# Kernel optimization log

Measured on AMD Instinct MI355X. Metric: run time of the kernel, lower is better.

Reference implementation:

```python
import jax, jax.numpy as jnp
import numpy as np

N_NODES = 50000
N_EDGES = 1600000
N_FEAT = 50
HID = 20
OUT_DIM = 10
N_GRAPHS = 64


def _glorot(key, shape):
    fan_in, fan_out = shape[0], shape[1]
    lim = float(np.sqrt(6.0 / (fan_in + fan_out)))
    return jax.random.uniform(key, shape, jnp.float32, -lim, lim)


def setup_inputs() -> dict:
    key = jax.random.key(0)
    ks = jax.random.split(key, 16)
    x = jax.random.normal(ks[0], (N_NODES, N_FEAT), jnp.float32)
    edge_index = jax.random.randint(ks[1], (2, N_EDGES), 0, N_NODES, jnp.int32)
    batch = jnp.sort(jax.random.randint(ks[2], (N_NODES,), 0, N_GRAPHS, jnp.int32))
    inp = {"x": x, "edge_index": edge_index, "batch": batch}
    # GraphConv layer params: lin_rel (weight+bias, applied to aggregated msgs), lin_root (no bias)
    dims = [(N_FEAT, HID), (HID, HID), (HID, HID)]
    for i, (di, do) in enumerate(dims, start=1):
        inp[f"W_rel{i}"] = _glorot(ks[3 * i], (di, do))
        inp[f"W_root{i}"] = _glorot(ks[3 * i + 1], (di, do))
        inp[f"b{i}"] = jnp.zeros((do,), jnp.float32)
    # final Linear on cat([max_pool, mean_pool]) -> in_features = 2*HID
    inp["W_lin"] = _glorot(ks[13], (2 * HID, OUT_DIM))
    inp["b_lin"] = jnp.zeros((OUT_DIM,), jnp.float32)
    return inp


def _graph_conv(x, src, dst, W_rel, W_root, b):
    # PyG GraphConv: aggregate raw neighbor features (sum), then linear.
    agg = jax.ops.segment_sum(x[src], dst, num_segments=N_NODES)  # [N, d_in]
    return agg @ W_rel + x @ W_root + b


def reference(x, edge_index, batch,
              W_rel1, W_root1, b1,
              W_rel2, W_root2, b2,
              W_rel3, W_root3, b3,
              W_lin, b_lin):
    src, dst = edge_index[0], edge_index[1]
    h = jax.nn.relu(_graph_conv(x, src, dst, W_rel1, W_root1, b1))
    h = jax.nn.relu(_graph_conv(h, src, dst, W_rel2, W_root2, b2))
    h = jax.nn.relu(_graph_conv(h, src, dst, W_rel3, W_root3, b3))
    # global max / mean pool per graph
    maxP = jax.ops.segment_max(h, batch, num_segments=N_GRAPHS)  # [G, HID]
    sums = jax.ops.segment_sum(h, batch, num_segments=N_GRAPHS)
    cnt = jax.ops.segment_sum(jnp.ones((h.shape[0], 1), h.dtype), batch, num_segments=N_GRAPHS)
    meanP = sums / jnp.maximum(cnt, 1.0)
    return jnp.concatenate([maxP, meanP], axis=-1) @ W_lin + b_lin
```

## Files before the change

### kernel.cpp

```cpp
#include <hip/hip_runtime.h>

#define N_NODES  50000
#define N_EDGES  1600000
#define N_FEAT   50
#define HID      20
#define OUT_DIM  10
#define N_GRAPHS 64

#define NBUCK 256
#define BCAP  8192
#define EPB   (N_EDGES/256)
#define YSTR  32
#define GEMMB 977

__device__ __forceinline__ int bstart(int b) { return (b * 65536 + 334) / 335; }


__global__ __launch_bounds__(1024) void k1_scatter_gemm(
        const int* __restrict__ dst, const int* __restrict__ srcv,
        int* __restrict__ gcur, unsigned int* __restrict__ padded,
        const float* __restrict__ x, const float* __restrict__ Wrel,
        const float* __restrict__ Wroot, const float* __restrict__ bb,
        float* __restrict__ y, float* __restrict__ acc,
        float* __restrict__ gmax, float* __restrict__ gsum, float* __restrict__ gcnt) {
    __shared__ char smem[14560];
    int t = threadIdx.x;
    if (blockIdx.x < 256) {
        unsigned short* rnk = (unsigned short*)smem;
        int* cnt   = (int*)(smem + 12512);
        int* gbase = cnt + 256;
        if (blockIdx.x == 0) {
            for (int i = t; i < N_GRAPHS * HID; i += 1024) { gmax[i] = 0.f; gsum[i] = 0.f; }
            if (t < N_GRAPHS) gcnt[t] = 0.f;
        }
        if (t < 256) cnt[t] = 0;
        __syncthreads();
        int e0 = blockIdx.x * EPB;
        for (int i = t; i < EPB; i += 1024) {
            unsigned int d = (unsigned int)dst[e0 + i];
            unsigned int key = (d * 335u) >> 16;
            rnk[i] = (unsigned short)atomicAdd(&cnt[key], 1);
        }
        __syncthreads();
        if (t < 256) gbase[t] = t * BCAP + atomicAdd(&gcur[t], cnt[t]);
        __syncthreads();
        for (int i = t; i < EPB; i += 1024) {
            unsigned int d = (unsigned int)dst[e0 + i];
            unsigned int s = (unsigned int)srcv[e0 + i];
            unsigned int key = (d * 335u) >> 16;
            int gp = gbase[key] + rnk[i];
            if (gp < (int)(key + 1) * BCAP) padded[gp] = (d << 16) | s;
        }
    } else {
        float* sWrel  = (float*)smem;
        float* sWroot = sWrel + N_FEAT * HID;
        for (int i = t; i < N_FEAT * HID; i += 1024) { sWrel[i] = Wrel[i]; sWroot[i] = Wroot[i]; }
        __syncthreads();
        int idx = (blockIdx.x - 256) * 1024 + t;
        if (idx < N_NODES * HID) {
            int n = idx / HID, j = idx % HID;
            const float* xr = x + n * N_FEAT;
            float a0 = 0.f, a1 = bb[j];
            #pragma unroll
            for (int k = 0; k < N_FEAT; ++k) {
                float xv = xr[k];
                a0 = fmaf(xv, sWrel[k * HID + j], a0);
                a1 = fmaf(xv, sWroot[k * HID + j], a1);
            }
            y[n * YSTR + j] = a0;
            acc[idx] = a1;
        }
    }
}


__global__ __launch_bounds__(1024) void k2_build_gather(
        const int* __restrict__ gcur, const unsigned int* __restrict__ padded,
        unsigned short* __restrict__ csr16, int* __restrict__ startg,
        int* __restrict__ cntg, unsigned short* __restrict__ permg,
        const float* __restrict__ y_in, const float* __restrict__ accp,
        const float* __restrict__ Wrel, const float* __restrict__ Wroot,
        const float* __restrict__ bb,
        float* __restrict__ y_out, float* __restrict__ acc_out) {
    __shared__ unsigned short eo[BCAP];
    __shared__ char uni[20480];
    __shared__ float sWrel[HID * HID], sWroot[HID * HID], sb[HID];
    __shared__ int cnt[256], scn[256], s_start[256], s_cnt[256];
    __shared__ unsigned short sperm[256];
    unsigned short* rnk = (unsigned short*)uni;
    float*          rh  = (float*)uni;
    int g = blockIdx.x, t = threadIdx.x;
    int base = g * BCAP;
    int m = min(gcur[g], BCAP);
    int n0 = bstart(g);
    int n1 = min(bstart(g + 1), N_NODES);
    int nvalid = n1 - n0;
    for (int i = t; i < HID * HID; i += 1024) { sWrel[i] = Wrel[i]; sWroot[i] = Wroot[i]; }
    if (t < HID) sb[t] = bb[t];
    if (t < 256) cnt[t] = 0;
    __syncthreads();
    for (int i = t; i < m; i += 1024) {
        int local = (int)(padded[base + i] >> 16) - n0;
        rnk[i] = (unsigned short)atomicAdd(&cnt[local], 1);
    }
    __syncthreads();
    if (t < 256) { s_cnt[t] = cnt[t]; scn[t] = cnt[t]; }
    __syncthreads();
    for (int d = 1; d < 256; d <<= 1) {
        int u = 0;
        if (t < 256 && t >= d) u = scn[t - d];
        __syncthreads();
        if (t < 256) scn[t] += u;
        __syncthreads();
    }
    if (t < 256) {
        s_start[t] = scn[t] - s_cnt[t];
        if (t < nvalid) { startg[n0 + t] = base + s_start[t]; cntg[n0 + t] = s_cnt[t]; }
    }
    __syncthreads();
    for (int i = t; i < m; i += 1024) {
        unsigned int e = padded[base + i];
        int local = (int)(e >> 16) - n0;
        eo[s_start[local] + rnk[i]] = (unsigned short)(e & 0xFFFFu);
    }
    __syncthreads();
    for (int i = t; i < m; i += 1024) csr16[base + i] = eo[i];
    if (t < 256) {
        int d = s_cnt[t], rank = 0;
        for (int j2 = 0; j2 < 256; ++j2) {
            int dj = s_cnt[j2];
            rank += (dj > d) || (dj == d && j2 < t);
        }
        sperm[rank] = (unsigned short)t;
    }
    __syncthreads();
    if (t < 256) permg[g * 256 + t] = sperm[t];
    for (int i = t; i < nvalid * HID; i += 1024) rh[i] = accp[n0 * HID + i];
    __syncthreads();
    int grp = t >> 3, lane = t & 7;
    if (lane < 5) {
        int q4 = lane * 4;
        #pragma unroll
        for (int rep = 0; rep < 2; ++rep) {
            int rank = rep ? 255 - grp : grp;
            int nl = sperm[rank];
            if (nl < nvalid) {
                int a = s_start[nl], e = a + s_cnt[nl];
                float4 s0 = make_float4(0.f, 0.f, 0.f, 0.f);
                float4 s1 = make_float4(0.f, 0.f, 0.f, 0.f);
                int k = a;
                for (; k + 3 < e; k += 4) {
                    int sn0 = eo[k], sn1 = eo[k + 1], sn2 = eo[k + 2], sn3 = eo[k + 3];
                    float4 v0 = *(const float4*)(y_in + sn0 * YSTR + q4);
                    float4 v1 = *(const float4*)(y_in + sn1 * YSTR + q4);
                    float4 v2 = *(const float4*)(y_in + sn2 * YSTR + q4);
                    float4 v3 = *(const float4*)(y_in + sn3 * YSTR + q4);
                    s0.x += v0.x + v2.x; s0.y += v0.y + v2.y;
                    s0.z += v0.z + v2.z; s0.w += v0.w + v2.w;
                    s1.x += v1.x + v3.x; s1.y += v1.y + v3.y;
                    s1.z += v1.z + v3.z; s1.w += v1.w + v3.w;
                }
                for (; k < e; ++k) {
                    int sn = eo[k];
                    float4 v = *(const float4*)(y_in + sn * YSTR + q4);
                    s0.x += v.x; s0.y += v.y; s0.z += v.z; s0.w += v.w;
                }
                float* rp = &rh[nl * HID + q4];
                rp[0] += s0.x + s1.x; rp[1] += s0.y + s1.y;
                rp[2] += s0.z + s1.z; rp[3] += s0.w + s1.w;
            }
        }
    }
    __syncthreads();
    for (int i = t; i < nvalid * 5; i += 1024) {
        int n = i / 5, j0 = (i % 5) * 4;
        float y0 = 0.f, y1 = 0.f, y2 = 0.f, y3 = 0.f;
        float a0 = sb[j0], a1 = sb[j0 + 1], a2 = sb[j0 + 2], a3 = sb[j0 + 3];
        #pragma unroll
        for (int k = 0; k < HID; ++k) {
            float h = fmaxf(rh[n * HID + k], 0.f);
            const float* wr = sWrel  + k * HID + j0;
            const float* wo = sWroot + k * HID + j0;
            y0 = fmaf(h, wr[0], y0); y1 = fmaf(h, wr[1], y1);
            y2 = fmaf(h, wr[2], y2); y3 = fmaf(h, wr[3], y3);
            a0 = fmaf(h, wo[0], a0); a1 = fmaf(h, wo[1], a1);
            a2 = fmaf(h, wo[2], a2); a3 = fmaf(h, wo[3], a3);
        }
        *(float4*)(y_out   + (n0 + n) * YSTR + j0) = make_float4(y0, y1, y2, y3);
        *(float4*)(acc_out + (n0 + n) * HID  + j0) = make_float4(a0, a1, a2, a3);
    }
}


__global__ __launch_bounds__(1024) void k3_gather_gemm(
        const int* __restrict__ startg, const int* __restrict__ cntg,
        const unsigned short* __restrict__ csr16, const unsigned short* __restrict__ permg,
        const float* __restrict__ y_in, const float* __restrict__ accp,
        const float* __restrict__ Wrel, const float* __restrict__ Wroot,
        const float* __restrict__ bb,
        float* __restrict__ y_out, float* __restrict__ acc_out) {
    __shared__ float rh[256 * HID];
    __shared__ float sWrel[HID * HID], sWroot[HID * HID], sb[HID];
    int g = blockIdx.x, t = threadIdx.x;
    int n0 = bstart(g);
    int n1 = min(bstart(g + 1), N_NODES);
    int nvalid = n1 - n0;
    for (int i = t; i < HID * HID; i += 1024) { sWrel[i] = Wrel[i]; sWroot[i] = Wroot[i]; }
    if (t < HID) sb[t] = bb[t];
    for (int i = t; i < nvalid * HID; i += 1024) rh[i] = accp[n0 * HID + i];
    __syncthreads();
    int grp = t >> 3, lane = t & 7;
    if (lane < 5) {
        int q4 = lane * 4;
        #pragma unroll
        for (int rep = 0; rep < 2; ++rep) {
            int rank = rep ? 255 - grp : grp;
            int nl = permg[g * 256 + rank];
            if (nl < nvalid) {
                int node = n0 + nl;
                int a = startg[node], e = a + cntg[node];
                float4 s0 = make_float4(0.f, 0.f, 0.f, 0.f);
                float4 s1 = make_float4(0.f, 0.f, 0.f, 0.f);
                int k = a;
                for (; k + 3 < e; k += 4) {
                    int sn0 = csr16[k], sn1 = csr16[k + 1], sn2 = csr16[k + 2], sn3 = csr16[k + 3];
                    float4 v0 = *(const float4*)(y_in + sn0 * YSTR + q4);
                    float4 v1 = *(const float4*)(y_in + sn1 * YSTR + q4);
                    float4 v2 = *(const float4*)(y_in + sn2 * YSTR + q4);
                    float4 v3 = *(const float4*)(y_in + sn3 * YSTR + q4);
                    s0.x += v0.x + v2.x; s0.y += v0.y + v2.y;
                    s0.z += v0.z + v2.z; s0.w += v0.w + v2.w;
                    s1.x += v1.x + v3.x; s1.y += v1.y + v3.y;
                    s1.z += v1.z + v3.z; s1.w += v1.w + v3.w;
                }
                for (; k < e; ++k) {
                    int sn = csr16[k];
                    float4 v = *(const float4*)(y_in + sn * YSTR + q4);
                    s0.x += v.x; s0.y += v.y; s0.z += v.z; s0.w += v.w;
                }
                float* rp = &rh[nl * HID + q4];
                rp[0] += s0.x + s1.x; rp[1] += s0.y + s1.y;
                rp[2] += s0.z + s1.z; rp[3] += s0.w + s1.w;
            }
        }
    }
    __syncthreads();
    for (int i = t; i < nvalid * 5; i += 1024) {
        int n = i / 5, j0 = (i % 5) * 4;
        float y0 = 0.f, y1 = 0.f, y2 = 0.f, y3 = 0.f;
        float a0 = sb[j0], a1 = sb[j0 + 1], a2 = sb[j0 + 2], a3 = sb[j0 + 3];
        #pragma unroll
        for (int k = 0; k < HID; ++k) {
            float h = fmaxf(rh[n * HID + k], 0.f);
            const float* wr = sWrel  + k * HID + j0;
            const float* wo = sWroot + k * HID + j0;
            y0 = fmaf(h, wr[0], y0); y1 = fmaf(h, wr[1], y1);
            y2 = fmaf(h, wr[2], y2); y3 = fmaf(h, wr[3], y3);
            a0 = fmaf(h, wo[0], a0); a1 = fmaf(h, wo[1], a1);
            a2 = fmaf(h, wo[2], a2); a3 = fmaf(h, wo[3], a3);
        }
        *(float4*)(y_out   + (n0 + n) * YSTR + j0) = make_float4(y0, y1, y2, y3);
        *(float4*)(acc_out + (n0 + n) * HID  + j0) = make_float4(a0, a1, a2, a3);
    }
}


__global__ __launch_bounds__(1024) void k4_gather_pool(
        const int* __restrict__ startg, const int* __restrict__ cntg,
        const unsigned short* __restrict__ csr16, const unsigned short* __restrict__ permg,
        const float* __restrict__ y_in, const float* __restrict__ accp,
        const int* __restrict__ batch,
        float* __restrict__ gmax, float* __restrict__ gsum, float* __restrict__ gcnt,
        int* __restrict__ done, const float* __restrict__ Wlin,
        const float* __restrict__ blin, float* __restrict__ out) {
    __shared__ float rh[256 * HID];
    __shared__ float redm[51 * HID], reds[51 * HID];
    __shared__ int sbatch[256];
    __shared__ int seglo[16], seghi[16];
    __shared__ int lastFlag;
    int g = blockIdx.x, t = threadIdx.x;
    int n0 = bstart(g);
    int n1 = min(bstart(g + 1), N_NODES);
    int nvalid = n1 - n0;
    for (int i = t; i < nvalid * HID; i += 1024) rh[i] = accp[n0 * HID + i];
    if (t < nvalid) sbatch[t] = batch[n0 + t];
    __syncthreads();
    int grp = t >> 3, lane = t & 7;
    if (lane < 5) {
        int q4 = lane * 4;
        #pragma unroll
        for (int rep = 0; rep < 2; ++rep) {
            int rank = rep ? 255 - grp : grp;
            int nl = permg[g * 256 + rank];
            if (nl < nvalid) {
                int node = n0 + nl;
                int a = startg[node], e = a + cntg[node];
                float4 s0 = make_float4(0.f, 0.f, 0.f, 0.f);
                float4 s1 = make_float4(0.f, 0.f, 0.f, 0.f);
                int k = a;
                for (; k + 3 < e; k += 4) {
                    int sn0 = csr16[k], sn1 = csr16[k + 1], sn2 = csr16[k + 2], sn3 = csr16[k + 3];
                    float4 v0 = *(const float4*)(y_in + sn0 * YSTR + q4);
                    float4 v1 = *(const float4*)(y_in + sn1 * YSTR + q4);
                    float4 v2 = *(const float4*)(y_in + sn2 * YSTR + q4);
                    float4 v3 = *(const float4*)(y_in + sn3 * YSTR + q4);
                    s0.x += v0.x + v2.x; s0.y += v0.y + v2.y;
                    s0.z += v0.z + v2.z; s0.w += v0.w + v2.w;
                    s1.x += v1.x + v3.x; s1.y += v1.y + v3.y;
                    s1.z += v1.z + v3.z; s1.w += v1.w + v3.w;
                }
                for (; k < e; ++k) {
                    int sn = csr16[k];
                    float4 v = *(const float4*)(y_in + sn * YSTR + q4);
                    s0.x += v.x; s0.y += v.y; s0.z += v.z; s0.w += v.w;
                }
                float* rp = &rh[nl * HID + q4];
                rp[0] += s0.x + s1.x; rp[1] += s0.y + s1.y;
                rp[2] += s0.z + s1.z; rp[3] += s0.w + s1.w;
            }
        }
    }
    __syncthreads();
    int g0 = sbatch[0];
    int span = sbatch[nvalid - 1] - g0 + 1;
    if (t < nvalid) {
        int bi = sbatch[t] - g0;
        if (bi < 16) {
            if (t == 0 || sbatch[t - 1] != sbatch[t]) seglo[bi] = t;
            if (t == nvalid - 1 || sbatch[t + 1] != sbatch[t]) seghi[bi] = t + 1;
        }
    }
    __syncthreads();
    if (span > 16) span = 16;
    for (int li = 0; li < span; ++li) {
        int lo = seglo[li], hi = seghi[li];
        int r = t / HID, j = t % HID;
        if (r < 51) {
            float mx = 0.f, sm = 0.f;
            for (int n = lo + r; n < hi; n += 51) {
                float v = fmaxf(rh[n * HID + j], 0.f);
                mx = fmaxf(mx, v); sm += v;
            }
            redm[r * HID + j] = mx; reds[r * HID + j] = sm;
        }
        __syncthreads();
        if (t < HID) {
            float mm = 0.f, ss = 0.f;
            #pragma unroll 17
            for (int r2 = 0; r2 < 51; ++r2) {
                mm = fmaxf(mm, redm[r2 * HID + t]);
                ss += reds[r2 * HID + t];
            }
            atomicMax((int*)&gmax[(g0 + li) * HID + t], __float_as_int(mm));
            atomicAdd(&gsum[(g0 + li) * HID + t], ss);
        }
        if (t == HID) atomicAdd(&gcnt[g0 + li], (float)(hi - lo));
        __syncthreads();
    }
    if (t == 0) {
        __threadfence();
        lastFlag = (atomicAdd(done, 1) == NBUCK - 1);
    }
    __syncthreads();
    if (!lastFlag) return;
    __threadfence();
    float* sW = redm;
    for (int i = t; i < 2 * HID * OUT_DIM; i += 1024) sW[i] = Wlin[i];
    __syncthreads();
    if (t < N_GRAPHS * OUT_DIM) {
        int gg = t / OUT_DIM, o = t % OUT_DIM;
        float c = fmaxf(gcnt[gg], 1.0f);
        float a = blin[o];
        #pragma unroll
        for (int j = 0; j < HID; ++j) {
            a = fmaf(gmax[gg * HID + j], sW[j * OUT_DIM + o], a);
            a = fmaf(gsum[gg * HID + j] / c, sW[(HID + j) * OUT_DIM + o], a);
        }
        out[t] = a;
    }
}

extern "C" void kernel_launch(void* const* d_in, const int* in_sizes, int n_in,
                              void* d_out, int out_size, void* d_ws, size_t ws_size,
                              hipStream_t stream) {
    const float* x      = (const float*)d_in[0];
    const int*   ei     = (const int*)  d_in[1];
    const int*   batch  = (const int*)  d_in[2];
    const float* Wrel1  = (const float*)d_in[3];
    const float* Wroot1 = (const float*)d_in[4];
    const float* b1     = (const float*)d_in[5];
    const float* Wrel2  = (const float*)d_in[6];
    const float* Wroot2 = (const float*)d_in[7];
    const float* b2     = (const float*)d_in[8];
    const float* Wrel3  = (const float*)d_in[9];
    const float* Wroot3 = (const float*)d_in[10];
    const float* b3     = (const float*)d_in[11];
    const float* Wlin   = (const float*)d_in[12];
    const float* blin   = (const float*)d_in[13];
    float* out = (float*)d_out;

    char* ws = (char*)d_ws;
    const size_t YB = (size_t)N_NODES * YSTR * sizeof(float);
    const size_t AB = (size_t)N_NODES * HID * sizeof(float);
    const size_t PB = (size_t)NBUCK * BCAP * sizeof(int);
    const size_t CB = (size_t)NBUCK * BCAP * sizeof(unsigned short);
    float*          yA     = (float*)(ws);
    float*          yB     = (float*)(ws + YB);
    float*          accA   = (float*)(ws + 2 * YB);
    float*          accB   = (float*)(ws + 2 * YB + AB);
    unsigned int*   padded = (unsigned int*)(ws + 2 * YB + 2 * AB);
    unsigned short* csr16  = (unsigned short*)(ws + 2 * YB + 2 * AB + PB);
    int*            startg = (int*)(ws + 2 * YB + 2 * AB + PB + CB);
    int*            cntg   = startg + N_NODES;
    unsigned short* permg  = (unsigned short*)(cntg + N_NODES);
    int*            gcur   = (int*)((char*)permg + (size_t)NBUCK * 256 * 2);
    int*            done   = gcur + NBUCK;
    float*          gmax   = (float*)(done + 4);
    float*          gsum   = gmax + N_GRAPHS * HID;
    float*          gcnt   = gsum + N_GRAPHS * HID;

    const int* src = ei;
    const int* dst = ei + N_EDGES;

    hipMemsetAsync(gcur, 0, (NBUCK + 1) * sizeof(int), stream);
    k1_scatter_gemm<<<256 + GEMMB, 1024, 0, stream>>>(dst, src, gcur, padded,
                                                      x, Wrel1, Wroot1, b1, yA, accA,
                                                      gmax, gsum, gcnt);
    k2_build_gather<<<NBUCK, 1024, 0, stream>>>(gcur, padded, csr16, startg, cntg, permg,
                                                yA, accA, Wrel2, Wroot2, b2, yB, accB);
    k3_gather_gemm<<<NBUCK, 1024, 0, stream>>>(startg, cntg, csr16, permg,
                                               yB, accB, Wrel3, Wroot3, b3, yA, accA);
    k4_gather_pool<<<NBUCK, 1024, 0, stream>>>(startg, cntg, csr16, permg,
                                               yA, accA, batch, gmax, gsum, gcnt,
                                               done, Wlin, blin, out);
}
```

Measured before the change: 122.3 us.

## Store gathered features as bf16, bucket by dst>>8, widen per-node gather threads

Intermediate y features used in neighbour gathers are now stored as bf16 (packed 20 values per row) instead of fp32, which halves the bytes read per edge in the gather kernels. Bucketing switches from a multiply-shift hash to plain 256-node buckets (dst>>8), with 196 buckets and a larger capacity. The scatter step first sorts edges locally in shared memory so global writes to the padded buffer are contiguous. The gather is restructured so each node's full 20-wide row is accumulated by 2 or 4 threads that split the edge list, with a shared-memory reduction afterwards. The cost is bf16 rounding error in the aggregated messages and more register pressure from the 20-float accumulator per thread.

```diff
diff --git a/kernel.cpp b/kernel.cpp
--- a/kernel.cpp
+++ b/kernel.cpp
@@ -7,13 +7,35 @@
 #define OUT_DIM  10
 #define N_GRAPHS 64
 
-#define NBUCK 256
-#define BCAP  8192
-#define EPB   (N_EDGES/256)
+#define NBUCK 196
+#define BCAP  10240
+#define EPB   6250
 #define YSTR  32
 #define GEMMB 977
 
-__device__ __forceinline__ int bstart(int b) { return (b * 65536 + 334) / 335; }
+__device__ __forceinline__ unsigned short f2bf(float f) {
+    unsigned int u = __float_as_uint(f);
+    u += 0x7FFFu + ((u >> 16) & 1u);
+    return (unsigned short)(u >> 16);
+}
+__device__ __forceinline__ unsigned int pk2(float f0, float f1) {
+    return (unsigned int)f2bf(f0) | ((unsigned int)f2bf(f1) << 16);
+}
+__device__ __forceinline__ float blo(unsigned int u) { return __uint_as_float(u << 16); }
+__device__ __forceinline__ float bhi(unsigned int u) { return __uint_as_float(u & 0xFFFF0000u); }
+
+__device__ __forceinline__ void addrow(const unsigned short* __restrict__ yb,
+                                       int sn, float* a) {
+    const unsigned short* p = yb + (size_t)sn * YSTR;
+    uint4 q0 = *(const uint4*)(p);
+    uint4 q1 = *(const uint4*)(p + 8);
+    uint2 q2 = *(const uint2*)(p + 16);
+    a[0] += blo(q0.x); a[1] += bhi(q0.x); a[2] += blo(q0.y); a[3] += bhi(q0.y);
+    a[4] += blo(q0.z); a[5] += bhi(q0.z); a[6] += blo(q0.w); a[7] += bhi(q0.w);
+    a[8] += blo(q1.x); a[9] += bhi(q1.x); a[10] += blo(q1.y); a[11] += bhi(q1.y);
+    a[12] += blo(q1.z); a[13] += bhi(q1.z); a[14] += blo(q1.w); a[15] += bhi(q1.w);
+    a[16] += blo(q2.x); a[17] += bhi(q2.x); a[18] += blo(q2.y); a[19] += bhi(q2.y);
+}
 
 
 __global__ __launch_bounds__(1024) void k1_scatter_gemm(
@@ -21,14 +43,17 @@
         int* __restrict__ gcur, unsigned int* __restrict__ padded,
         const float* __restrict__ x, const float* __restrict__ Wrel,
         const float* __restrict__ Wroot, const float* __restrict__ bb,
-        float* __restrict__ y, float* __restrict__ acc,
+        unsigned short* __restrict__ y, float* __restrict__ acc,
         float* __restrict__ gmax, float* __restrict__ gsum, float* __restrict__ gcnt) {
-    __shared__ char smem[14560];
+    __shared__ char smem[41728];
     int t = threadIdx.x;
     if (blockIdx.x < 256) {
         unsigned short* rnk = (unsigned short*)smem;
-        int* cnt   = (int*)(smem + 12512);
-        int* gbase = cnt + 256;
+        unsigned int*   ep2 = (unsigned int*)(smem + 12544);
+        int* cnt   = (int*)(smem + 37632);
+        int* scn   = cnt + 256;
+        int* lofs  = scn + 256;
+        int* gbase = lofs + 256;
         if (blockIdx.x == 0) {
             for (int i = t; i < N_GRAPHS * HID; i += 1024) { gmax[i] = 0.f; gsum[i] = 0.f; }
             if (t < N_GRAPHS) gcnt[t] = 0.f;
@@ -37,19 +62,33 @@
         __syncthreads();
         int e0 = blockIdx.x * EPB;
         for (int i = t; i < EPB; i += 1024) {
-            unsigned int d = (unsigned int)dst[e0 + i];
-            unsigned int key = (d * 335u) >> 16;
-            rnk[i] = (unsigned short)atomicAdd(&cnt[key], 1);
-        }
-        __syncthreads();
-        if (t < 256) gbase[t] = t * BCAP + atomicAdd(&gcur[t], cnt[t]);
+            int d = dst[e0 + i];
+            rnk[i] = (unsigned short)atomicAdd(&cnt[d >> 8], 1);
+        }
+        __syncthreads();
+        if (t < 256) scn[t] = cnt[t];
+        __syncthreads();
+        for (int d = 1; d < 256; d <<= 1) {
+            int u = 0;
+            if (t < 256 && t >= d) u = scn[t - d];
+            __syncthreads();
+            if (t < 256) scn[t] += u;
+            __syncthreads();
+        }
+        if (t < 256) lofs[t] = scn[t] - cnt[t];
+        if (t < NBUCK) gbase[t] = t * BCAP + atomicAdd(&gcur[t], cnt[t]);
         __syncthreads();
         for (int i = t; i < EPB; i += 1024) {
             unsigned int d = (unsigned int)dst[e0 + i];
             unsigned int s = (unsigned int)srcv[e0 + i];
-            unsigned int key = (d * 335u) >> 16;
-            int gp = gbase[key] + rnk[i];
-            if (gp < (int)(key + 1) * BCAP) padded[gp] = (d << 16) | s;
+            ep2[lofs[d >> 8] + rnk[i]] = (d << 16) | s;
+        }
+        __syncthreads();
+        for (int i = t; i < EPB; i += 1024) {
+            unsigned int e = ep2[i];
+            int bk = e >> 24;
+            int gp = gbase[bk] + (i - lofs[bk]);
+            if (gp < (bk + 1) * BCAP) padded[gp] = e;
         }
     } else {
         float* sWrel  = (float*)smem;
@@ -67,7 +106,7 @@
                 a0 = fmaf(xv, sWrel[k * HID + j], a0);
                 a1 = fmaf(xv, sWroot[k * HID + j], a1);
             }
-            y[n * YSTR + j] = a0;
+            y[(size_t)n * YSTR + j] = f2bf(a0);
             acc[idx] = a1;
         }
     }
@@ -78,10 +117,10 @@
         const int* __restrict__ gcur, const unsigned int* __restrict__ padded,
         unsigned short* __restrict__ csr16, int* __restrict__ startg,
         int* __restrict__ cntg, unsigned short* __restrict__ permg,
-        const float* __restrict__ y_in, const float* __restrict__ accp,
+        const unsigned short* __restrict__ y_in, const float* __restrict__ accp,
         const float* __restrict__ Wrel, const float* __restrict__ Wroot,
         const float* __restrict__ bb,
-        float* __restrict__ y_out, float* __restrict__ acc_out) {
+        unsigned short* __restrict__ y_out, float* __restrict__ acc_out) {
     __shared__ unsigned short eo[BCAP];
     __shared__ char uni[20480];
     __shared__ float sWrel[HID * HID], sWroot[HID * HID], sb[HID];
@@ -92,15 +131,14 @@
     int g = blockIdx.x, t = threadIdx.x;
     int base = g * BCAP;
     int m = min(gcur[g], BCAP);
-    int n0 = bstart(g);
-    int n1 = min(bstart(g + 1), N_NODES);
-    int nvalid = n1 - n0;
+    int n0 = g * 256;
+    int nvalid = min(256, N_NODES - n0);
     for (int i = t; i < HID * HID; i += 1024) { sWrel[i] = Wrel[i]; sWroot[i] = Wroot[i]; }
     if (t < HID) sb[t] = bb[t];
     if (t < 256) cnt[t] = 0;
     __syncthreads();
     for (int i = t; i < m; i += 1024) {
-        int local = (int)(padded[base + i] >> 16) - n0;
+        int local = (padded[base + i] >> 16) & 255;
         rnk[i] = (unsigned short)atomicAdd(&cnt[local], 1);
     }
     __syncthreads();
@@ -120,7 +158,7 @@
     __syncthreads();
     for (int i = t; i < m; i += 1024) {
         unsigned int e = padded[base + i];
-        int local = (int)(e >> 16) - n0;
+        int local = (e >> 16) & 255;
         eo[s_start[local] + rnk[i]] = (unsigned short)(e & 0xFFFFu);
     }
     __syncthreads();
@@ -135,47 +173,49 @@
     }
     __syncthreads();
     if (t < 256) permg[g * 256 + t] = sperm[t];
-    for (int i = t; i < nvalid * HID; i += 1024) rh[i] = accp[n0 * HID + i];
-    __syncthreads();
-    int grp = t >> 3, lane = t & 7;
-    if (lane < 5) {
-        int q4 = lane * 4;
-        #pragma unroll
-        for (int rep = 0; rep < 2; ++rep) {
-            int rank = rep ? 255 - grp : grp;
-            int nl = sperm[rank];
-            if (nl < nvalid) {
-                int a = s_start[nl], e = a + s_cnt[nl];
-                float4 s0 = make_float4(0.f, 0.f, 0.f, 0.f);
-                float4 s1 = make_float4(0.f, 0.f, 0.f, 0.f);
-                int k = a;
-                for (; k + 3 < e; k += 4) {
-                    int sn0 = eo[k], sn1 = eo[k + 1], sn2 = eo[k + 2], sn3 = eo[k + 3];
-                    float4 v0 = *(const float4*)(y_in + sn0 * YSTR + q4);
-                    float4 v1 = *(const float4*)(y_in + sn1 * YSTR + q4);
-                    float4 v2 = *(const float4*)(y_in + sn2 * YSTR + q4);
-                    float4 v3 = *(const float4*)(y_in + sn3 * YSTR + q4);
-                    s0.x += v0.x + v2.x; s0.y += v0.y + v2.y;
-                    s0.z += v0.z + v2.z; s0.w += v0.w + v2.w;
-                    s1.x += v1.x + v3.x; s1.y += v1.y + v3.y;
-                    s1.z += v1.z + v3.z; s1.w += v1.w + v3.w;
-                }
-                for (; k < e; ++k) {
-                    int sn = eo[k];
-                    float4 v = *(const float4*)(y_in + sn * YSTR + q4);
-                    s0.x += v.x; s0.y += v.y; s0.z += v.z; s0.w += v.w;
-                }
-                float* rp = &rh[nl * HID + q4];
-                rp[0] += s0.x + s1.x; rp[1] += s0.y + s1.y;
-                rp[2] += s0.z + s1.z; rp[3] += s0.w + s1.w;
-            }
+    bool act = t < 512;
+    int slot = t >> 1, half = t & 1;
+    float a[HID];
+    #pragma unroll
+    for (int j = 0; j < HID; ++j) a[j] = 0.f;
+    int nl = 0; bool ok = false; int a0 = 0, cn = 0;
+    if (act) {
+        nl = sperm[slot];
+        ok = nl < nvalid;
+        if (ok) { a0 = s_start[nl]; cn = s_cnt[nl]; }
+    }
+    if (ok) {
+        #pragma unroll 2
+        for (int k = half; k < cn; k += 2) addrow(y_in, eo[a0 + k], a);
+        if (half == 0) {
+            const float4* ar = (const float4*)(accp + (size_t)(n0 + nl) * HID);
+            #pragma unroll
+            for (int q = 0; q < 5; ++q) {
+                float4 v = ar[q];
+                a[q*4+0] += v.x; a[q*4+1] += v.y; a[q*4+2] += v.z; a[q*4+3] += v.w;
+            }
+        }
+    }
+    if (ok && half == 0) {
+        #pragma unroll
+        for (int q = 0; q < 5; ++q)
+            *(float4*)&rh[nl * HID + q * 4] =
+                make_float4(a[q*4], a[q*4+1], a[q*4+2], a[q*4+3]);
+    }
+    __syncthreads();
+    if (ok && half == 1) {
+        #pragma unroll
+        for (int q = 0; q < 5; ++q) {
+            float4 v = *(float4*)&rh[nl * HID + q * 4];
+            v.x += a[q*4]; v.y += a[q*4+1]; v.z += a[q*4+2]; v.w += a[q*4+3];
+            *(float4*)&rh[nl * HID + q * 4] = v;
         }
     }
     __syncthreads();
     for (int i = t; i < nvalid * 5; i += 1024) {
         int n = i / 5, j0 = (i % 5) * 4;
         float y0 = 0.f, y1 = 0.f, y2 = 0.f, y3 = 0.f;
-        float a0 = sb[j0], a1 = sb[j0 + 1], a2 = sb[j0 + 2], a3 = sb[j0 + 3];
+        float c0 = sb[j0], c1 = sb[j0+1], c2 = sb[j0+2], c3 = sb[j0+3];
         #pragma unroll
         for (int k = 0; k < HID; ++k) {
             float h = fmaxf(rh[n * HID + k], 0.f);
@@ -183,11 +223,11 @@
             const float* wo = sWroot + k * HID + j0;
             y0 = fmaf(h, wr[0], y0); y1 = fmaf(h, wr[1], y1);
             y2 = fmaf(h, wr[2], y2); y3 = fmaf(h, wr[3], y3);
-            a0 = fmaf(h, wo[0], a0); a1 = fmaf(h, wo[1], a1);
-            a2 = fmaf(h, wo[2], a2); a3 = fmaf(h, wo[3], a3);
-        }
-        *(float4*)(y_out   + (n0 + n) * YSTR + j0) = make_float4(y0, y1, y2, y3);
-        *(float4*)(acc_out + (n0 + n) * HID  + j0) = make_float4(a0, a1, a2, a3);
+            c0 = fmaf(h, wo[0], c0); c1 = fmaf(h, wo[1], c1);
+            c2 = fmaf(h, wo[2], c2); c3 = fmaf(h, wo[3], c3);
+        }
+        *(uint2*)(y_out + (size_t)(n0 + n) * YSTR + j0) = make_uint2(pk2(y0, y1), pk2(y2, y3));
+        *(float4*)(acc_out + (size_t)(n0 + n) * HID + j0) = make_float4(c0, c1, c2, c3);
     }
 }
 
@@ -195,72 +235,75 @@
 __global__ __launch_bounds__(1024) void k3_gather_gemm(
         const int* __restrict__ startg, const int* __restrict__ cntg,
         const unsigned short* __restrict__ csr16, const unsigned short* __restrict__ permg,
-        const float* __restrict__ y_in, const float* __restrict__ accp,
+        const unsigned short* __restrict__ y_in, const float* __restrict__ accp,
         const float* __restrict__ Wrel, const float* __restrict__ Wroot,
         const float* __restrict__ bb,
-        float* __restrict__ y_out, float* __restrict__ acc_out) {
+        unsigned short* __restrict__ y_out, float* __restrict__ acc_out) {
     __shared__ float rh[256 * HID];
+    __shared__ float rh2[256 * HID];
     __shared__ float sWrel[HID * HID], sWroot[HID * HID], sb[HID];
+    __shared__ unsigned short sperm[256];
     int g = blockIdx.x, t = threadIdx.x;
-    int n0 = bstart(g);
-    int n1 = min(bstart(g + 1), N_NODES);
-    int nvalid = n1 - n0;
+    int n0 = g * 256;
+    int nvalid = min(256, N_NODES - n0);
     for (int i = t; i < HID * HID; i += 1024) { sWrel[i] = Wrel[i]; sWroot[i] = Wroot[i]; }
     if (t < HID) sb[t] = bb[t];
-    for (int i = t; i < nvalid * HID; i += 1024) rh[i] = accp[n0 * HID + i];
-    __syncthreads();
-    int grp = t >> 3, lane = t & 7;
-    if (lane < 5) {
-        int q4 = lane * 4;
-        #pragma unroll
-        for (int rep = 0; rep < 2; ++rep) {
-            int rank = rep ? 255 - grp : grp;
-            int nl = permg[g * 256 + rank];
-            if (nl < nvalid) {
-                int node = n0 + nl;
-                int a = startg[node], e = a + cntg[node];
-                float4 s0 = make_float4(0.f, 0.f, 0.f, 0.f);
-                float4 s1 = make_float4(0.f, 0.f, 0.f, 0.f);
-                int k = a;
-                for (; k + 3 < e; k += 4) {
-                    int sn0 = csr16[k], sn1 = csr16[k + 1], sn2 = csr16[k + 2], sn3 = csr16[k + 3];
-                    float4 v0 = *(const float4*)(y_in + sn0 * YSTR + q4);
-                    float4 v1 = *(const float4*)(y_in + sn1 * YSTR + q4);
-                    float4 v2 = *(const float4*)(y_in + sn2 * YSTR + q4);
-                    float4 v3 = *(const float4*)(y_in + sn3 * YSTR + q4);
-                    s0.x += v0.x + v2.x; s0.y += v0.y + v2.y;
-                    s0.z += v0.z + v2.z; s0.w += v0.w + v2.w;
-                    s1.x += v1.x + v3.x; s1.y += v1.y + v3.y;
-                    s1.z += v1.z + v3.z; s1.w += v1.w + v3.w;
-                }
-                for (; k < e; ++k) {
-                    int sn = csr16[k];
-                    float4 v = *(const float4*)(y_in + sn * YSTR + q4);
-                    s0.x += v.x; s0.y += v.y; s0.z += v.z; s0.w += v.w;
-                }
-                float* rp = &rh[nl * HID + q4];
-                rp[0] += s0.x + s1.x; rp[1] += s0.y + s1.y;
-                rp[2] += s0.z + s1.z; rp[3] += s0.w + s1.w;
-            }
+    if (t < 256) sperm[t] = permg[g * 256 + t];
+    __syncthreads();
+    int slot = t >> 2, q = t & 3;
+    int nl = sperm[slot];
+    bool ok = nl < nvalid;
+    float a[HID];
+    #pragma unroll
+    for (int j = 0; j < HID; ++j) a[j] = 0.f;
+    if (ok) {
+        int node = n0 + nl;
+        int a0 = startg[node], cn = cntg[node];
+        #pragma unroll 2
+        for (int k = q; k < cn; k += 4) addrow(y_in, csr16[a0 + k], a);
+        if (q == 0) {
+            const float4* ar = (const float4*)(accp + (size_t)node * HID);
+            #pragma unroll
+            for (int qq = 0; qq < 5; ++qq) {
+                float4 v = ar[qq];
+                a[qq*4+0] += v.x; a[qq*4+1] += v.y; a[qq*4+2] += v.z; a[qq*4+3] += v.w;
+            }
+        }
+    }
+    if (ok && (q == 0 || q == 2)) {
+        float* dstp = (q == 0) ? rh : rh2;
+        #pragma unroll
+        for (int qq = 0; qq < 5; ++qq)
+            *(float4*)&dstp[nl * HID + qq * 4] =
+                make_float4(a[qq*4], a[qq*4+1], a[qq*4+2], a[qq*4+3]);
+    }
+    __syncthreads();
+    if (ok && (q == 1 || q == 3)) {
+        float* dstp = (q == 1) ? rh : rh2;
+        #pragma unroll
+        for (int qq = 0; qq < 5; ++qq) {
+            float4 v = *(float4*)&dstp[nl * HID + qq * 4];
+            v.x += a[qq*4]; v.y += a[qq*4+1]; v.z += a[qq*4+2]; v.w += a[qq*4+3];
+            *(float4*)&dstp[nl * HID + qq * 4] = v;
         }
     }
     __syncthreads();
     for (int i = t; i < nvalid * 5; i += 1024) {
         int n = i / 5, j0 = (i % 5) * 4;
         float y0 = 0.f, y1 = 0.f, y2 = 0.f, y3 = 0.f;
-        float a0 = sb[j0], a1 = sb[j0 + 1], a2 = sb[j0 + 2], a3 = sb[j0 + 3];
+        float c0 = sb[j0], c1 = sb[j0+1], c2 = sb[j0+2], c3 = sb[j0+3];
         #pragma unroll
         for (int k = 0; k < HID; ++k) {
-            float h = fmaxf(rh[n * HID + k], 0.f);
+            float h = fmaxf(rh[n * HID + k] + rh2[n * HID + k], 0.f);
             const float* wr = sWrel  + k * HID + j0;
             const float* wo = sWroot + k * HID + j0;
             y0 = fmaf(h, wr[0], y0); y1 = fmaf(h, wr[1], y1);
             y2 = fmaf(h, wr[2], y2); y3 = fmaf(h, wr[3], y3);
-            a0 = fmaf(h, wo[0], a0); a1 = fmaf(h, wo[1], a1);
-            a2 = fmaf(h, wo[2], a2); a3 = fmaf(h, wo[3], a3);
-        }
-        *(float4*)(y_out   + (n0 + n) * YSTR + j0) = make_float4(y0, y1, y2, y3);
-        *(float4*)(acc_out + (n0 + n) * HID  + j0) = make_float4(a0, a1, a2, a3);
+            c0 = fmaf(h, wo[0], c0); c1 = fmaf(h, wo[1], c1);
+            c2 = fmaf(h, wo[2], c2); c3 = fmaf(h, wo[3], c3);
+        }
+        *(uint2*)(y_out + (size_t)(n0 + n) * YSTR + j0) = make_uint2(pk2(y0, y1), pk2(y2, y3));
+        *(float4*)(acc_out + (size_t)(n0 + n) * HID + j0) = make_float4(c0, c1, c2, c3);
     }
 }
 
@@ -268,56 +311,59 @@
 __global__ __launch_bounds__(1024) void k4_gather_pool(
         const int* __restrict__ startg, const int* __restrict__ cntg,
         const unsigned short* __restrict__ csr16, const unsigned short* __restrict__ permg,
-        const float* __restrict__ y_in, const float* __restrict__ accp,
+        const unsigned short* __restrict__ y_in, const float* __restrict__ accp,
         const int* __restrict__ batch,
         float* __restrict__ gmax, float* __restrict__ gsum, float* __restrict__ gcnt,
         int* __restrict__ done, const float* __restrict__ Wlin,
         const float* __restrict__ blin, float* __restrict__ out) {
     __shared__ float rh[256 * HID];
+    __shared__ float rh2[256 * HID];
     __shared__ float redm[51 * HID], reds[51 * HID];
+    __shared__ unsigned short sperm[256];
     __shared__ int sbatch[256];
     __shared__ int seglo[16], seghi[16];
     __shared__ int lastFlag;
     int g = blockIdx.x, t = threadIdx.x;
-    int n0 = bstart(g);
-    int n1 = min(bstart(g + 1), N_NODES);
-    int nvalid = n1 - n0;
-    for (int i = t; i < nvalid * HID; i += 1024) rh[i] = accp[n0 * HID + i];
+    int n0 = g * 256;
+    int nvalid = min(256, N_NODES - n0);
+    if (t < 256) sperm[t] = permg[g * 256 + t];
     if (t < nvalid) sbatch[t] = batch[n0 + t];
     __syncthreads();
-    int grp = t >> 3, lane = t & 7;
-    if (lane < 5) {
-        int q4 = lane * 4;
-        #pragma unroll
-        for (int rep = 0; rep < 2; ++rep) {
-            int rank = rep ? 255 - grp : grp;
-            int nl = permg[g * 256 + rank];
-            if (nl < nvalid) {
-                int node = n0 + nl;
-                int a = startg[node], e = a + cntg[node];
-                float4 s0 = make_float4(0.f, 0.f, 0.f, 0.f);
-                float4 s1 = make_float4(0.f, 0.f, 0.f, 0.f);
-                int k = a;
-                for (; k + 3 < e; k += 4) {
-                    int sn0 = csr16[k], sn1 = csr16[k + 1], sn2 = csr16[k + 2], sn3 = csr16[k + 3];
-                    float4 v0 = *(const float4*)(y_in + sn0 * YSTR + q4);
-                    float4 v1 = *(const float4*)(y_in + sn1 * YSTR + q4);
-                    float4 v2 = *(const float4*)(y_in + sn2 * YSTR + q4);
-                    float4 v3 = *(const float4*)(y_in + sn3 * YSTR + q4);
-                    s0.x += v0.x + v2.x; s0.y += v0.y + v2.y;
-                    s0.z += v0.z + v2.z; s0.w += v0.w + v2.w;
-                    s1.x += v1.x + v3.x; s1.y += v1.y + v3.y;
-                    s1.z += v1.z + v3.z; s1.w += v1.w + v3.w;
-                }
-                for (; k < e; ++k) {
-                    int sn = csr16[k];
-                    float4 v = *(const float4*)(y_in + sn * YSTR + q4);
-                    s0.x += v.x; s0.y += v.y; s0.z += v.z; s0.w += v.w;
-                }
-                float* rp = &rh[nl * HID + q4];
-                rp[0] += s0.x + s1.x; rp[1] += s0.y + s1.y;
-                rp[2] += s0.z + s1.z; rp[3] += s0.w + s1.w;
-            }
+    int slot = t >> 2, q = t & 3;
+    int nl = sperm[slot];
+    bool ok = nl < nvalid;
+    float a[HID];
+    #pragma unroll
+    for (int j = 0; j < HID; ++j) a[j] = 0.f;
+    if (ok) {
+        int node = n0 + nl;
+        int a0 = startg[node], cn = cntg[node];
+        #pragma unroll 2
+        for (int k = q; k < cn; k += 4) addrow(y_in, csr16[a0 + k], a);
+        if (q == 0) {
+            const float4* ar = (const float4*)(accp + (size_t)node * HID);
+            #pragma unroll
+            for (int qq = 0; qq < 5; ++qq) {
+                float4 v = ar[qq];
+                a[qq*4+0] += v.x; a[qq*4+1] += v.y; a[qq*4+2] += v.z; a[qq*4+3] += v.w;
+            }
+        }
+    }
+    if (ok && (q == 0 || q == 2)) {
+        float* dstp = (q == 0) ? rh : rh2;
+        #pragma unroll
+        for (int qq = 0; qq < 5; ++qq)
+            *(float4*)&dstp[nl * HID + qq * 4] =
+                make_float4(a[qq*4], a[qq*4+1], a[qq*4+2], a[qq*4+3]);
+    }
+    __syncthreads();
+    if (ok && (q == 1 || q == 3)) {
+        float* dstp = (q == 1) ? rh : rh2;
+        #pragma unroll
+        for (int qq = 0; qq < 5; ++qq) {
+            float4 v = *(float4*)&dstp[nl * HID + qq * 4];
+            v.x += a[qq*4]; v.y += a[qq*4+1]; v.z += a[qq*4+2]; v.w += a[qq*4+3];
+            *(float4*)&dstp[nl * HID + qq * 4] = v;
         }
     }
     __syncthreads();
@@ -338,7 +384,7 @@
         if (r < 51) {
             float mx = 0.f, sm = 0.f;
             for (int n = lo + r; n < hi; n += 51) {
-                float v = fmaxf(rh[n * HID + j], 0.f);
+                float v = fmaxf(rh[n * HID + j] + rh2[n * HID + j], 0.f);
                 mx = fmaxf(mx, v); sm += v;
             }
             redm[r * HID + j] = mx; reds[r * HID + j] = sm;
@@ -370,13 +416,13 @@
     if (t < N_GRAPHS * OUT_DIM) {
         int gg = t / OUT_DIM, o = t % OUT_DIM;
         float c = fmaxf(gcnt[gg], 1.0f);
-        float a = blin[o];
+        float av = blin[o];
         #pragma unroll
         for (int j = 0; j < HID; ++j) {
-            a = fmaf(gmax[gg * HID + j], sW[j * OUT_DIM + o], a);
-            a = fmaf(gsum[gg * HID + j] / c, sW[(HID + j) * OUT_DIM + o], a);
-        }
-        out[t] = a;
+            av = fmaf(gmax[gg * HID + j], sW[j * OUT_DIM + o], av);
+            av = fmaf(gsum[gg * HID + j] / c, sW[(HID + j) * OUT_DIM + o], av);
+        }
+        out[t] = av;
     }
 }
 
@@ -400,20 +446,21 @@
     float* out = (float*)d_out;
 
     char* ws = (char*)d_ws;
-    const size_t YB = (size_t)N_NODES * YSTR * sizeof(float);
-    const size_t AB = (size_t)N_NODES * HID * sizeof(float);
-    const size_t PB = (size_t)NBUCK * BCAP * sizeof(int);
-    const size_t CB = (size_t)NBUCK * BCAP * sizeof(unsigned short);
-    float*          yA     = (float*)(ws);
-    float*          yB     = (float*)(ws + YB);
+    const size_t YB = (size_t)N_NODES * YSTR * 2;
+    const size_t AB = (size_t)N_NODES * HID * 4;
+    const size_t PB = (size_t)NBUCK * BCAP * 4;
+    const size_t CB = (size_t)NBUCK * BCAP * 2;
+    const size_t NP = (size_t)NBUCK * 256;
+    unsigned short* yA     = (unsigned short*)(ws);
+    unsigned short* yB     = (unsigned short*)(ws + YB);
     float*          accA   = (float*)(ws + 2 * YB);
     float*          accB   = (float*)(ws + 2 * YB + AB);
     unsigned int*   padded = (unsigned int*)(ws + 2 * YB + 2 * AB);
     unsigned short* csr16  = (unsigned short*)(ws + 2 * YB + 2 * AB + PB);
     int*            startg = (int*)(ws + 2 * YB + 2 * AB + PB + CB);
-    int*            cntg   = startg + N_NODES;
-    unsigned short* permg  = (unsigned short*)(cntg + N_NODES);
-    int*            gcur   = (int*)((char*)permg + (size_t)NBUCK * 256 * 2);
+    int*            cntg   = startg + NP;
+    unsigned short* permg  = (unsigned short*)(cntg + NP);
+    int*            gcur   = (int*)((char*)permg + NP * 2);
     int*            done   = gcur + NBUCK;
     float*          gmax   = (float*)(done + 4);
     float*          gsum   = gmax + N_GRAPHS * HID;
```

New measurement: 117.2 us. 4.2% less time.
